# Kernel optimization log

Hardware: AMD Instinct MI355X
Metric: run time of the kernel (lower is better)

Reference implementation:

```python
import jax, jax.numpy as jnp
import numpy as np

DIM = 768
HEADS = 12
HEAD_DIM = DIM // HEADS  # 64, must equal 2*ROPE_DIM
HIDDEN = int(DIM * 4 * 2 / 3)  # 2048
EPS = 1e-6


def _ln(x, w, b, eps=EPS):
    mu = jnp.mean(x, -1, keepdims=True)
    var = jnp.mean((x - mu) ** 2, -1, keepdims=True)
    return (x - mu) * jax.lax.rsqrt(var + eps) * w + b


def _rotate_half(x):
    xr = x.reshape(x.shape[:-1] + (-1, 2))
    return jnp.stack((-xr[..., 1], xr[..., 0]), -1).reshape(x.shape)


def _rope_tables(H, W):
    # Matches get_rope: dim=32 per axis, pt_seq_len=16, theta=10000
    dim, pt, theta = 32, 16.0, 10000.0
    freqs = 1.0 / theta ** (np.arange(0, dim, 2, dtype=np.float32) / dim)  # [16]
    fH = np.repeat((np.arange(H, dtype=np.float32) / H * pt)[:, None] * freqs[None, :], 2, axis=-1)  # [H,32]
    fW = np.repeat((np.arange(W, dtype=np.float32) / W * pt)[:, None] * freqs[None, :], 2, axis=-1)  # [W,32]
    f = np.concatenate([np.broadcast_to(fH[:, None, :], (H, W, dim)),
                        np.broadcast_to(fW[None, :, :], (H, W, dim))], -1)  # [H,W,64]
    f = f.reshape(H * W, 2 * dim)
    return jnp.asarray(np.cos(f)), jnp.asarray(np.sin(f))


def block_forward(x, ln1_w, ln1_b, q_w, q_b, k_w, v_w, v_b, proj_w, proj_b,
                  ln2_w, ln2_b, w1_w, w1_b, w2_w, w2_b, ffn_w, ffn_b, w3_w, w3_b, ws):
    B, H, W, C = x.shape
    shortcut = x
    h = _ln(x, ln1_w, ln1_b)
    # window partition with padding
    pad_h = (-H) % ws
    pad_w = (-W) % ws
    h = jnp.pad(h, ((0, 0), (0, pad_h), (0, pad_w), (0, 0)))
    Hp, Wp = H + pad_h, W + pad_w
    h = h.reshape(B, Hp // ws, ws, Wp // ws, ws, C).transpose(0, 1, 3, 2, 4, 5).reshape(-1, ws, ws, C)
    Bw = h.shape[0]
    N = ws * ws
    t = h.reshape(Bw, N, C)
    q = t @ q_w + q_b  # k has no bias
    k = t @ k_w
    v = t @ v_w + v_b
    q = q.reshape(Bw, N, HEADS, HEAD_DIM).transpose(0, 2, 1, 3)  # [Bw,h,N,d]
    k = k.reshape(Bw, N, HEADS, HEAD_DIM).transpose(0, 2, 1, 3)
    v = v.reshape(Bw, N, HEADS, HEAD_DIM).transpose(0, 2, 1, 3)
    cos, sin = _rope_tables(ws, ws)  # [N, 64]
    q = q * cos + _rotate_half(q) * sin
    k = k * cos + _rotate_half(k) * sin
    scale = HEAD_DIM ** (-0.5)
    attn = jax.nn.softmax(jnp.einsum('bhnd,bhmd->bhnm', q * scale, k), axis=-1)
    o = jnp.einsum('bhnm,bhmd->bhnd', attn, v).transpose(0, 2, 1, 3).reshape(Bw, N, -1)
    o = o @ proj_w + proj_b
    o = o.reshape(Bw, ws, ws, C)
    # window unpartition
    o = o.reshape(B, Hp // ws, Wp // ws, ws, ws, C).transpose(0, 1, 3, 2, 4, 5).reshape(B, Hp, Wp, C)
    o = o[:, :H, :W, :]
    x = shortcut + o
    # SwiGLU MLP with sub-LN
    h = _ln(x, ln2_w, ln2_b)
    hid = jax.nn.silu(h @ w1_w + w1_b) * (h @ w2_w + w2_b)
    hid = _ln(hid, ffn_w, ffn_b)
    return x + hid @ w3_w + w3_b


def setup_inputs() -> dict:
    key = jax.random.key(0)
    ks = jax.random.split(key, 9)
    s = 0.02
    d = {
        'x': jax.random.normal(ks[0], (8, 64, 64, DIM), jnp.float32),
        'ln1_w': jnp.ones((DIM,), jnp.float32),
        'ln1_b': jnp.zeros((DIM,), jnp.float32),
        'q_w': jax.random.normal(ks[1], (DIM, DIM), jnp.float32) * s,
        'q_b': jnp.zeros((DIM,), jnp.float32),
        'k_w': jax.random.normal(ks[2], (DIM, DIM), jnp.float32) * s,
        'v_w': jax.random.normal(ks[3], (DIM, DIM), jnp.float32) * s,
        'v_b': jnp.zeros((DIM,), jnp.float32),
        'proj_w': jax.random.normal(ks[4], (DIM, DIM), jnp.float32) * s,
        'proj_b': jnp.zeros((DIM,), jnp.float32),
        'ln2_w': jnp.ones((DIM,), jnp.float32),
        'ln2_b': jnp.zeros((DIM,), jnp.float32),
        'w1_w': jax.random.normal(ks[5], (DIM, HIDDEN), jnp.float32) * s,
        'w1_b': jnp.zeros((HIDDEN,), jnp.float32),
        'w2_w': jax.random.normal(ks[6], (DIM, HIDDEN), jnp.float32) * s,
        'w2_b': jnp.zeros((HIDDEN,), jnp.float32),
        'ffn_w': jnp.ones((HIDDEN,), jnp.float32),
        'ffn_b': jnp.zeros((HIDDEN,), jnp.float32),
        'w3_w': jax.random.normal(ks[7], (HIDDEN, DIM), jnp.float32) * s,
        'w3_b': jnp.zeros((DIM,), jnp.float32),
        'window_size': 14,
    }
    return d


def reference(x, ln1_w, ln1_b, q_w, q_b, k_w, v_w, v_b, proj_w, proj_b,
              ln2_w, ln2_b, w1_w, w1_b, w2_w, w2_b, ffn_w, ffn_b, w3_w, w3_b, window_size):
    return block_forward(x, ln1_w, ln1_b, q_w, q_b, k_w, v_w, v_b, proj_w, proj_b,
                         ln2_w, ln2_b, w1_w, w1_b, w2_w, w2_b, ffn_w, ffn_b, w3_w, w3_b,
                         int(window_size))
```

## Files before the change

kernel.cpp:

```cpp
#include <hip/hip_runtime.h>
#include <hip/hip_bf16.h>
#include <stdint.h>

typedef unsigned short u16;
typedef unsigned int u32;
typedef __attribute__((ext_vector_type(4))) float f32x4;
typedef __attribute__((ext_vector_type(8))) short s16x8;
typedef __attribute__((ext_vector_type(4))) u32 u32x4;

#define DEV __device__ __forceinline__
#define AS1 __attribute__((address_space(1)))
#define AS3 __attribute__((address_space(3)))

constexpr int T2 = 8 * 64 * 64;
constexpr int C = 768;
constexpr int HID = 2048;
constexpr int CHUNK = 8192;
constexpr int QKVS = 2304;

DEV float blo(u32 u) { return __uint_as_float(u << 16); }
DEV float bhi(u32 u) { return __uint_as_float(u & 0xffff0000u); }
DEV float b2f(u16 u) { return __uint_as_float((u32)u << 16); }
DEV u16 f2bf(float f) {
  u32 x = __float_as_uint(f);
  u32 r = x + 0x7fffu + ((x >> 16) & 1u);
  return (u16)(r >> 16);
}
DEV u32 pack2(float a, float b) { return (u32)f2bf(a) | ((u32)f2bf(b) << 16); }
DEV u32 cvtpk(float lo, float hi) {
  u32 r;
  asm("v_cvt_pk_bf16_f32 %0, %1, %2" : "=v"(r) : "v"(lo), "v"(hi));
  return r;
}

template <int NW>
DEV void reduce2(float& s, float& q) {
#pragma unroll
  for (int o = 32; o > 0; o >>= 1) {
    s += __shfl_down(s, o);
    q += __shfl_down(q, o);
  }
  __shared__ float ps[2 * NW];
  int wave = threadIdx.x >> 6, lane = threadIdx.x & 63;
  if (lane == 0) { ps[wave] = s; ps[NW + wave] = q; }
  __syncthreads();
  s = 0.f; q = 0.f;
#pragma unroll
  for (int i = 0; i < NW; ++i) { s += ps[i]; q += ps[NW + i]; }
}

__global__ __launch_bounds__(256) void transpose_cvt_tiled_k(
    const float* __restrict__ src, u16* __restrict__ dst, int K, int N, int rs, int ro) {
  __shared__ float t[32][33];
  int k0 = blockIdx.x * 32, n0 = blockIdx.y * 32;
  int tx = threadIdx.x, ty = threadIdx.y;
#pragma unroll
  for (int j = 0; j < 4; ++j)
    t[ty + j * 8][tx] = src[(size_t)(k0 + ty + j * 8) * N + n0 + tx];
  __syncthreads();
#pragma unroll
  for (int j = 0; j < 4; ++j) {
    int n = n0 + ty + j * 8;
    dst[((size_t)n * rs + ro) * K + k0 + tx] = f2bf(t[tx][ty + j * 8]);
  }
}

__global__ void build_biases_k(const float* __restrict__ qb, const float* __restrict__ vbb,
                               const float* __restrict__ w1b, const float* __restrict__ w2b,
                               float* __restrict__ qkvb, float* __restrict__ w12b) {
  int i = blockIdx.x * 256 + threadIdx.x;
  if (i < 2304)
    qkvb[i] = i < 768 ? qb[i] : (i < 1536 ? 0.f : vbb[i - 1536]);
  int j = i - 2304;
  if (j >= 0 && j < 4096) w12b[j] = (j & 1) ? w2b[j >> 1] : w1b[j >> 1];
}

__global__ void rope_tables_k(float2* __restrict__ csp) {
  int i = blockIdx.x * 256 + threadIdx.x;
  if (i >= 196 * 32) return;
  int n = i >> 5, dp = i & 31;
  int r = n / 14, c = n - r * 14;
  float pos, fj;
  if (dp < 16) { pos = (float)r * (16.f / 14.f); fj = (float)dp; }
  else         { pos = (float)c * (16.f / 14.f); fj = (float)(dp - 16); }
  float fr = __expf(fj * (-2.f / 32.f) * logf(10000.f));
  float ang = pos * fr;
  csp[i] = make_float2(cosf(ang), sinf(ang));
}

__global__ __launch_bounds__(256) void ln_k(const float* __restrict__ in,
    const float* __restrict__ w, const float* __restrict__ bb, u16* __restrict__ out) {
  size_t row = blockIdx.x;
  int tid = threadIdx.x;
  const float* xr = in + row * C;
  float v0 = xr[tid], v1 = xr[tid + 256], v2 = xr[tid + 512];
  float s = v0 + v1 + v2, q = v0 * v0 + v1 * v1 + v2 * v2;
  reduce2<4>(s, q);
  float mu = s * (1.f / 768.f), var = q * (1.f / 768.f) - mu * mu;
  float rs = rsqrtf(var + 1e-6f);
  u16* orow = out + row * C;
  orow[tid]       = f2bf((v0 - mu) * rs * w[tid]       + bb[tid]);
  orow[tid + 256] = f2bf((v1 - mu) * rs * w[tid + 256] + bb[tid + 256]);
  orow[tid + 512] = f2bf((v2 - mu) * rs * w[tid + 512] + bb[tid + 512]);
}

__global__ __launch_bounds__(384) void ln_bf16_k(const u16* __restrict__ in,
    const float* __restrict__ w, const float* __restrict__ bb, u16* __restrict__ out) {
  size_t row = blockIdx.x;
  int t = threadIdx.x;
  u32 u = ((const u32*)(in + row * C))[t];
  float v0 = blo(u), v1 = bhi(u);
  float s = v0 + v1, q = v0 * v0 + v1 * v1;
  reduce2<6>(s, q);
  float mu = s * (1.f / 768.f), var = q * (1.f / 768.f) - mu * mu;
  float rs = rsqrtf(var + 1e-6f);
  float o0 = (v0 - mu) * rs * w[2 * t] + bb[2 * t];
  float o1 = (v1 - mu) * rs * w[2 * t + 1] + bb[2 * t + 1];
  ((u32*)(out + row * C))[t] = cvtpk(o0, o1);
}

template <int EPI>
__global__ __launch_bounds__(512, 2) void gemm256_k(
    const u16* __restrict__ A, const u16* __restrict__ Bt,
    const float* __restrict__ bias, void* __restrict__ Cout,
    const void* __restrict__ resid, int M, int Nn, int K, int lda,
    const float2* __restrict__ csp) {
  __shared__ u16 LDS[65536];
  const int tid = threadIdx.x;
  const int wave = tid >> 6, lane = tid & 63;
  const int wm = wave >> 2, wn = wave & 3;
  const int l16 = lane & 15, lq = lane >> 4;
  const int gx = gridDim.x;
  const int id = blockIdx.y * gx + blockIdx.x;
  const int xcd = id & 7;
  const int j0 = id >> 3;
  const int W = gx >> 3;
  const int SW = W < 8 ? W : 8;
  const int per_sub = gridDim.y * SW;
  const int sub = j0 / per_sub;
  const int jj = j0 - sub * per_sub;
  const int tm = xcd * W + sub * SW + (jj & (SW - 1));
  const int tn = jj / SW;

  f32x4 acc[8][4];
#pragma unroll
  for (int a = 0; a < 8; ++a)
#pragma unroll
    for (int b = 0; b < 4; ++b)
#pragma unroll
      for (int e = 0; e < 4; ++e) acc[a][b][e] = 0.f;

  const int nk = K >> 6;
  auto STAGE = [&](int kt, int buf) {
    const int k0 = kt << 6;
    u16* Ad = LDS + buf * 32768;
    u16* Bd = Ad + 16384;
#pragma unroll
    for (int i = 0; i < 4; ++i) {
      int blk = (wave << 2) + i;
      int row = (blk << 3) + (lane >> 3);
      int cl = (lane & 7) ^ (row & 7);
      const u16* sa = A + (size_t)(tm * 256 + row) * lda + k0 + cl * 8;
      __builtin_amdgcn_global_load_lds((const AS1 u32*)sa, (AS3 u32*)(Ad + (blk << 9)),
                                       16, 0, 0);
      const u16* sb = Bt + (size_t)(tn * 256 + row) * K + k0 + cl * 8;
      __builtin_amdgcn_global_load_lds((const AS1 u32*)sb, (AS3 u32*)(Bd + (blk << 9)),
                                       16, 0, 0);
    }
  };

  STAGE(0, 0);
  asm volatile("s_waitcnt vmcnt(0)" ::: "memory");
  __syncthreads();
  for (int t = 0; t < nk; ++t) {
    const int cur = t & 1;
    if (t + 1 < nk) STAGE(t + 1, cur ^ 1);
    const u16* As = LDS + cur * 32768;
    const u16* Bs = As + 16384;
#pragma unroll
    for (int ks = 0; ks < 2; ++ks) {
      s16x8 bfr[4];
#pragma unroll
      for (int nf = 0; nf < 4; ++nf) {
        int row = (wn << 6) + (nf << 4) + l16;
        int sc = ((ks << 2) + lq) ^ (row & 7);
        bfr[nf] = *(const s16x8*)(Bs + row * 64 + sc * 8);
      }
      __builtin_amdgcn_s_setprio(1);
#pragma unroll
      for (int mf = 0; mf < 8; ++mf) {
        int row = (wm << 7) + (mf << 4) + l16;
        int sc = ((ks << 2) + lq) ^ (row & 7);
        s16x8 af = *(const s16x8*)(As + row * 64 + sc * 8);
#pragma unroll
        for (int nf = 0; nf < 4; ++nf)
          acc[mf][nf] =
              __builtin_amdgcn_mfma_f32_16x16x32_bf16(af, bfr[nf], acc[mf][nf], 0, 0, 0);
      }
      __builtin_amdgcn_s_setprio(0);
    }
    asm volatile("s_waitcnt vmcnt(0)" ::: "memory");
    __syncthreads();
  }

#pragma unroll
  for (int nf = 0; nf < 4; ++nf) {
    int lcol = (wn << 6) + (nf << 4) + l16;
    int col = (tn << 8) + lcol;
    float bs = bias[col];
#pragma unroll
    for (int mf = 0; mf < 8; ++mf) {
      int rloc = (wm << 7) + (mf << 4) + (lq << 2);
      float v[4];
#pragma unroll
      for (int j = 0; j < 4; ++j) v[j] = acc[mf][nf][j] + bs;
      if constexpr (EPI == 1) {
        const float* rp = (const float*)resid;
#pragma unroll
        for (int j = 0; j < 4; ++j)
          v[j] += rp[(size_t)(tm * 256 + rloc + j) * Nn + col];
      }
#pragma unroll
      for (int j = 0; j < 4; ++j) {
        int row = rloc + j;
        int byte = row * 512 + ((lcol * 2) ^ ((row & 7) << 4));
        *(u16*)((char*)LDS + byte) = f2bf(v[j]);
      }
    }
  }
  __syncthreads();
  u16* Cb = (u16*)Cout + (size_t)(tm * 256) * Nn + (tn << 8);
  const int chunk = tid & 31;
  const int cbase = (tn << 8) + chunk * 8;
  const bool inqk = cbase < 1536, isq = cbase < 768;
  const int dp0 = (cbase & 63) >> 1;
#pragma unroll
  for (int it = 0; it < 16; ++it) {
    int row = (tid >> 5) + it * 16;
    int byte = row * 512 + ((chunk * 16) ^ ((row & 7) << 4));
    u32x4 val = *(const u32x4*)((const char*)LDS + byte);
    if constexpr (EPI == 3) {
      if (inqk) {
        int tok = tm * 256 + row;
        int rem = tok & 4095;
        int n = ((rem >> 6) % 14) * 14 + ((rem & 63) % 14);
        const float2* cp = csp + n * 32 + dp0;
        u32 wv[4] = {val.x, val.y, val.z, val.w};
#pragma unroll
        for (int p = 0; p < 4; ++p) {
          float2 cs = cp[p];
          float e = blo(wv[p]), o = bhi(wv[p]);
          float re = e * cs.x - o * cs.y;
          float ro = o * cs.x + e * cs.y;
          if (isq) { re *= 0.125f; ro *= 0.125f; }
          wv[p] = cvtpk(re, ro);
        }
        val = (u32x4){wv[0], wv[1], wv[2], wv[3]};
      }
    }
    *(u32x4*)(Cb + (size_t)row * Nn + chunk * 8) = val;
  }
}

__global__ __launch_bounds__(256) void gemm_k(
    const u16* __restrict__ A, const u16* __restrict__ Bt,
    const float* __restrict__ bias, float* __restrict__ Cout,
    const u16* __restrict__ resid, int M, int Nn, int K, int lda) {
  __shared__ u16 As[128 * 64];
  __shared__ u16 Bs[128 * 64];
  const int tid = threadIdx.x;
  const int wave = tid >> 6, lane = tid & 63;
  const int wm = wave >> 1, wn = wave & 1;
  const int gx = gridDim.x;
  const int id = blockIdx.y * gx + blockIdx.x;
  const int xcd = id & 7;
  const int j0 = id >> 3;
  const int W = gx >> 3;
  const int SW = W < 8 ? W : 8;
  const int per_sub = gridDim.y * SW;
  const int sub = j0 / per_sub;
  const int jj = j0 - sub * per_sub;
  const int tm = xcd * W + sub * SW + (jj & (SW - 1));
  const int tn = jj / SW;
  const int l16 = lane & 15, lq = lane >> 4;

  f32x4 acc[4][4];
#pragma unroll
  for (int a = 0; a < 4; ++a)
#pragma unroll
    for (int b = 0; b < 4; ++b)
#pragma unroll
      for (int e = 0; e < 4; ++e) acc[a][b][e] = 0.f;

  const int nk = K >> 6;
  for (int kt = 0; kt < nk; ++kt) {
    const int k0 = kt << 6;
#pragma unroll
    for (int i = 0; i < 4; ++i) {
      int row = (((wave << 2) + i) << 3) + (lane >> 3);
      int cl = (lane & 7) ^ (row & 7);
      const u16* sa = A + (size_t)(tm * 128 + row) * lda + k0 + cl * 8;
      __builtin_amdgcn_global_load_lds((const AS1 u32*)sa,
          (AS3 u32*)(As + (((wave << 2) + i) << 9)), 16, 0, 0);
      const u16* sb = Bt + (size_t)(tn * 128 + row) * K + k0 + cl * 8;
      __builtin_amdgcn_global_load_lds((const AS1 u32*)sb,
          (AS3 u32*)(Bs + (((wave << 2) + i) << 9)), 16, 0, 0);
    }
    asm volatile("s_waitcnt vmcnt(0)" ::: "memory");
    __syncthreads();
#pragma unroll
    for (int ks = 0; ks < 2; ++ks) {
      s16x8 af[4], bfr[4];
#pragma unroll
      for (int mf = 0; mf < 4; ++mf) {
        int row = (wm << 6) + (mf << 4) + l16;
        int sc = ((ks << 2) + lq) ^ (row & 7);
        af[mf] = *(const s16x8*)(As + row * 64 + sc * 8);
      }
#pragma unroll
      for (int nf = 0; nf < 4; ++nf) {
        int row = (wn << 6) + (nf << 4) + l16;
        int sc = ((ks << 2) + lq) ^ (row & 7);
        bfr[nf] = *(const s16x8*)(Bs + row * 64 + sc * 8);
      }
      __builtin_amdgcn_s_setprio(1);
#pragma unroll
      for (int mf = 0; mf < 4; ++mf)
#pragma unroll
        for (int nf = 0; nf < 4; ++nf)
          acc[mf][nf] =
              __builtin_amdgcn_mfma_f32_16x16x32_bf16(af[mf], bfr[nf], acc[mf][nf], 0, 0, 0);
      __builtin_amdgcn_s_setprio(0);
    }
    __syncthreads();
  }
#pragma unroll
  for (int nf = 0; nf < 4; ++nf) {
    int col = (tn << 7) + (wn << 6) + (nf << 4) + l16;
    float bs = bias[col];
#pragma unroll
    for (int mf = 0; mf < 4; ++mf) {
      int rbase = (tm << 7) + (wm << 6) + (mf << 4) + (lq << 2);
#pragma unroll
      for (int j = 0; j < 4; ++j) {
        size_t idx = (size_t)(rbase + j) * Nn + col;
        __builtin_nontemporal_store(b2f(resid[idx]) + acc[mf][nf][j] + bs, &Cout[idx]);
      }
    }
  }
}

__global__ __launch_bounds__(256) void attn_mfma_k(u16* __restrict__ qkv,
    const float* __restrict__ vb) {
  __shared__ u16 Vt[64 * 224];
  __shared__ u16 Pl[4 * 16 * 40];
  __shared__ int rowTab[208];
  int wid = blockIdx.x / 12, h = blockIdx.x - wid * 12;
  int bi = wid / 25, wr = wid - bi * 25;
  int hi = wr / 5, wj = wr - hi * 5;
  int rh = (hi == 4) ? 8 : 14, rw = (wj == 4) ? 8 : 14;
  int nv = rh * rw;
  int nk16 = (nv + 15) >> 4;
  int kvfull = nk16 >> 1;
  int nsteps = kvfull + (nk16 & 1);
  int vcols = ((nk16 + 1) >> 1) << 5;
  int tid = threadIdx.x;
  int rowbase = (bi * 64 + hi * 14) * 64 + wj * 14;

  if (tid < 208) {
    int mk = tid < nv ? tid : nv - 1;
    int nr = mk / rw, nc = mk - nr * rw;
    rowTab[tid] = rowbase + nr * 64 + nc;
  }
  __syncthreads();
  for (int idx = tid; idx < vcols * 32; idx += 256) {
    int key = idx >> 5, dp = idx & 31;
    int d = dp << 1;
    u32 val;
    if (key < nv) {
      size_t off = (size_t)rowTab[key] * QKVS + 1536 + (h << 6) + d;
      val = *(const u32*)(qkv + off);
    } else {
      val = pack2(vb[(h << 6) + d], vb[(h << 6) + d + 1]);
    }
    int b0 = (d * 448 + key * 2) ^ ((d & 7) << 4);
    int b1 = ((d + 1) * 448 + key * 2) ^ (((d + 1) & 7) << 4);
    Vt[b0 >> 1] = (u16)(val & 0xffffu);
    Vt[b1 >> 1] = (u16)(val >> 16);
  }
  __syncthreads();

  int wave = tid >> 6, lane = tid & 63;
  int l16 = lane & 15, lq = lane >> 4;
  u16* Pw = Pl + wave * 640;
  const u16* kbase = qkv + 768 + (h << 6);
  float vbr[4];
#pragma unroll
  for (int dt = 0; dt < 4; ++dt) vbr[dt] = vb[(h << 6) + dt * 16 + l16];

  int mtiles = (nv + 15) >> 4;
  for (int mt = wave; mt < mtiles; mt += 4) {
    s16x8 a[2];
    {
      int qi = mt * 16 + l16;
      const u16* qp = qkv + (size_t)rowTab[qi] * QKVS + (h << 6);
      a[0] = *(const s16x8*)(qp + lq * 8);
      a[1] = *(const s16x8*)(qp + 32 + lq * 8);
    }
    f32x4 O[4];
#pragma unroll
    for (int dt = 0; dt < 4; ++dt)
#pragma unroll
      for (int j = 0; j < 4; ++j) O[dt][j] = 0.f;
    float lrow[4] = {0.f, 0.f, 0.f, 0.f};

    for (int kv = 0; kv < nsteps; ++kv) {
      const bool full = kv < kvfull;
      const int keyb = kv << 5;
      f32x4 s0 = {0.f, 0.f, 0.f, 0.f}, s1 = {0.f, 0.f, 0.f, 0.f};
      int key0 = keyb + l16, key1 = key0 + 16;
      const u16* kr0 = kbase + (size_t)rowTab[key0] * QKVS;
      const u16* kr1 = full ? (kbase + (size_t)rowTab[key1] * QKVS) : kbase;
      __builtin_amdgcn_s_setprio(1);
#pragma unroll
      for (int s = 0; s < 2; ++s) {
        s16x8 b0 = *(const s16x8*)(kr0 + s * 32 + lq * 8);
        s0 = __builtin_amdgcn_mfma_f32_16x16x32_bf16(a[s], b0, s0, 0, 0, 0);
        if (full) {
          s16x8 b1 = *(const s16x8*)(kr1 + s * 32 + lq * 8);
          s1 = __builtin_amdgcn_mfma_f32_16x16x32_bf16(a[s], b1, s1, 0, 0, 0);
        }
      }
      __builtin_amdgcn_s_setprio(0);
#pragma unroll
      for (int j = 0; j < 4; ++j) {
        float p0 = key0 < nv ? __expf(s0[j]) : (key0 < 196 ? 1.f : 0.f);
        float p1 = full ? (key1 < nv ? __expf(s1[j]) : (key1 < 196 ? 1.f : 0.f)) : 0.f;
        float rs = p0 + p1;
        rs += __shfl_xor(rs, 1);
        rs += __shfl_xor(rs, 2);
        rs += __shfl_xor(rs, 4);
        rs += __shfl_xor(rs, 8);
        lrow[j] += rs;
        u32 pk = cvtpk(p0, p1);
        Pw[(lq * 4 + j) * 40 + l16] = (u16)pk;
        Pw[(lq * 4 + j) * 40 + l16 + 16] = (u16)(pk >> 16);
      }
      s16x8 pa = *(const s16x8*)(Pw + l16 * 40 + lq * 8);
      __builtin_amdgcn_s_setprio(1);
#pragma unroll
      for (int dt = 0; dt < 4; ++dt) {
        int d = dt * 16 + l16;
        int vbyte = (d * 448 + keyb * 2 + lq * 16) ^ ((d & 7) << 4);
        s16x8 bv = *(const s16x8*)(Vt + (vbyte >> 1));
        O[dt] = __builtin_amdgcn_mfma_f32_16x16x32_bf16(pa, bv, O[dt], 0, 0, 0);
      }
      __builtin_amdgcn_s_setprio(0);
    }
    int Prem = 196 - (nk16 << 4);
    if (Prem > 0) {
#pragma unroll
      for (int j = 0; j < 4; ++j) {
        lrow[j] += (float)Prem;
#pragma unroll
        for (int dt = 0; dt < 4; ++dt) O[dt][j] += (float)Prem * vbr[dt];
      }
    }
#pragma unroll
    for (int j = 0; j < 4; ++j) {
      int qi = mt * 16 + lq * 4 + j;
      if (qi < nv) {
        float inv = 1.f / lrow[j];
        u16* op = qkv + (size_t)rowTab[qi] * QKVS + (h << 6);
#pragma unroll
        for (int dt = 0; dt < 4; ++dt) op[dt * 16 + l16] = f2bf(O[dt][j] * inv);
      }
    }
  }
}

__global__ __launch_bounds__(256) void swiglu_ln_k(u16* __restrict__ h12,
    const float* __restrict__ w, const float* __restrict__ bb) {
  size_t row = blockIdx.x;
  int tid = threadIdx.x;
  const u32x4 ua = *(const u32x4*)(h12 + row * 4096 + tid * 16);
  const u32x4 ub = *(const u32x4*)(h12 + row * 4096 + tid * 16 + 8);
  u32 pp[8] = {ua.x, ua.y, ua.z, ua.w, ub.x, ub.y, ub.z, ub.w};
  float g[8];
  float s = 0.f, qq = 0.f;
#pragma unroll
  for (int j = 0; j < 8; ++j) {
    float a = blo(pp[j]), b = bhi(pp[j]);
    float sl = a / (1.f + __expf(-a));
    g[j] = sl * b;
    s += g[j];
    qq += g[j] * g[j];
  }
  reduce2<4>(s, qq);
  float mu = s * (1.f / 2048.f);
  float var = qq * (1.f / 2048.f) - mu * mu;
  float rs = rsqrtf(var + 1e-6f);
  const float* wp = w + tid * 8;
  const float* bp = bb + tid * 8;
  u32 o4[4];
#pragma unroll
  for (int j = 0; j < 4; ++j) {
    float o0 = (g[2 * j] - mu) * rs * wp[2 * j] + bp[2 * j];
    float o1 = (g[2 * j + 1] - mu) * rs * wp[2 * j + 1] + bp[2 * j + 1];
    o4[j] = cvtpk(o0, o1);
  }
  *(u32x4*)(h12 + row * 4096 + tid * 8) = (u32x4){o4[0], o4[1], o4[2], o4[3]};
}

extern "C" void kernel_launch(void* const* d_in, const int* in_sizes, int n_in,
                              void* d_out, int out_size, void* d_ws, size_t ws_size,
                              hipStream_t stream) {
  const float* x    = (const float*)d_in[0];
  const float* ln1w = (const float*)d_in[1];
  const float* ln1b = (const float*)d_in[2];
  const float* qw   = (const float*)d_in[3];
  const float* qb   = (const float*)d_in[4];
  const float* kw   = (const float*)d_in[5];
  const float* vw   = (const float*)d_in[6];
  const float* vb   = (const float*)d_in[7];
  const float* pw   = (const float*)d_in[8];
  const float* pb   = (const float*)d_in[9];
  const float* ln2w = (const float*)d_in[10];
  const float* ln2b = (const float*)d_in[11];
  const float* w1   = (const float*)d_in[12];
  const float* w1b  = (const float*)d_in[13];
  const float* w2   = (const float*)d_in[14];
  const float* w2b  = (const float*)d_in[15];
  const float* ffw  = (const float*)d_in[16];
  const float* ffb  = (const float*)d_in[17];
  const float* w3   = (const float*)d_in[18];
  const float* w3b  = (const float*)d_in[19];

  char* ws = (char*)d_ws;
  size_t off = 0;
  auto alloc = [&](size_t bytes) -> char* {
    char* p = ws + off;
    off += (bytes + 255) & ~(size_t)255;
    return p;
  };
  u16* qkvwt = (u16*)alloc((size_t)QKVS * 768 * 2);
  u16* pwt   = (u16*)alloc((size_t)768 * 768 * 2);
  u16* w12t  = (u16*)alloc((size_t)4096 * 768 * 2);
  u16* w3t   = (u16*)alloc((size_t)768 * 2048 * 2);
  float* qkvb = (float*)alloc((size_t)QKVS * 4);
  float* w12b = (float*)alloc((size_t)4096 * 4);
  float2* csp = (float2*)alloc((size_t)196 * 32 * 8);
  u16* xw  = (u16*)alloc((size_t)T2 * C * 2);
  u16* qkv = (u16*)alloc((size_t)T2 * QKVS * 2);
  u16* x2b  = xw;
  u16* h2   = qkv;
  u16* h12c = qkv + (size_t)T2 * C;
  float* outp = (float*)d_out;

  dim3 tb(32, 8);
  transpose_cvt_tiled_k<<<dim3(24, 24), tb, 0, stream>>>(qw, qkvwt, 768, 768, 1, 0);
  transpose_cvt_tiled_k<<<dim3(24, 24), tb, 0, stream>>>(kw, qkvwt + (size_t)768 * 768, 768, 768, 1, 0);
  transpose_cvt_tiled_k<<<dim3(24, 24), tb, 0, stream>>>(vw, qkvwt + (size_t)1536 * 768, 768, 768, 1, 0);
  transpose_cvt_tiled_k<<<dim3(24, 24), tb, 0, stream>>>(pw, pwt, 768, 768, 1, 0);
  transpose_cvt_tiled_k<<<dim3(24, 64), tb, 0, stream>>>(w1, w12t, 768, 2048, 2, 0);
  transpose_cvt_tiled_k<<<dim3(24, 64), tb, 0, stream>>>(w2, w12t, 768, 2048, 2, 1);
  transpose_cvt_tiled_k<<<dim3(64, 24), tb, 0, stream>>>(w3, w3t, 2048, 768, 1, 0);
  build_biases_k<<<25, 256, 0, stream>>>(qb, vb, w1b, w2b, qkvb, w12b);
  rope_tables_k<<<25, 256, 0, stream>>>(csp);

  ln_k<<<T2, 256, 0, stream>>>(x, ln1w, ln1b, xw);
  gemm256_k<3><<<dim3(T2 / 256, QKVS / 256), 512, 0, stream>>>(
      xw, qkvwt, qkvb, qkv, nullptr, T2, QKVS, 768, 768, csp);
  attn_mfma_k<<<200 * 12, 256, 0, stream>>>(qkv, vb);
  gemm256_k<1><<<dim3(T2 / 256, 3), 512, 0, stream>>>(
      qkv, pwt, pb, x2b, x, T2, 768, 768, QKVS, nullptr);

  ln_bf16_k<<<T2, 384, 0, stream>>>(x2b, ln2w, ln2b, h2);
  for (int cidx = 0; cidx < T2 / CHUNK; ++cidx) {
    const u16* hrow = h2 + (size_t)cidx * CHUNK * C;
    gemm256_k<0><<<dim3(CHUNK / 256, 16), 512, 0, stream>>>(
        hrow, w12t, w12b, h12c, nullptr, CHUNK, 4096, 768, 768, nullptr);
    swiglu_ln_k<<<CHUNK, 256, 0, stream>>>(h12c, ffw, ffb);
    gemm_k<<<dim3(CHUNK / 128, 6), 256, 0, stream>>>(
        h12c, w3t, w3b, outp + (size_t)cidx * CHUNK * C,
        x2b + (size_t)cidx * CHUNK * C, CHUNK, 768, 2048, 4096);
  }
}
```

Baseline: 924.3 us.

## Drop GEMM double buffering and halve LDS to raise occupancy

The 256x256 GEMM now uses a single LDS buffer instead of double buffering, so shared memory halves. The launch bound asks for four blocks per CU. The epilogue is staged in two 128-row passes to fit the smaller LDS. This gives up overlap between global loads and MFMA compute in the hope of more resident blocks, and risks register spills under the tighter bound.

```diff
diff --git a/kernel.cpp b/kernel.cpp
--- a/kernel.cpp
+++ b/kernel.cpp
@@ -120,12 +120,12 @@
 }
 
 template <int EPI>
-__global__ __launch_bounds__(512, 2) void gemm256_k(
+__global__ __launch_bounds__(512, 4) void gemm256_k(
     const u16* __restrict__ A, const u16* __restrict__ Bt,
     const float* __restrict__ bias, void* __restrict__ Cout,
     const void* __restrict__ resid, int M, int Nn, int K, int lda,
     const float2* __restrict__ csp) {
-  __shared__ u16 LDS[65536];
+  __shared__ u16 LDS[32768];
   const int tid = threadIdx.x;
   const int wave = tid >> 6, lane = tid & 63;
   const int wm = wave >> 2, wn = wave & 3;
@@ -151,32 +151,28 @@
       for (int e = 0; e < 4; ++e) acc[a][b][e] = 0.f;
 
   const int nk = K >> 6;
-  auto STAGE = [&](int kt, int buf) {
-    const int k0 = kt << 6;
-    u16* Ad = LDS + buf * 32768;
-    u16* Bd = Ad + 16384;
-#pragma unroll
-    for (int i = 0; i < 4; ++i) {
-      int blk = (wave << 2) + i;
-      int row = (blk << 3) + (lane >> 3);
-      int cl = (lane & 7) ^ (row & 7);
-      const u16* sa = A + (size_t)(tm * 256 + row) * lda + k0 + cl * 8;
-      __builtin_amdgcn_global_load_lds((const AS1 u32*)sa, (AS3 u32*)(Ad + (blk << 9)),
-                                       16, 0, 0);
-      const u16* sb = Bt + (size_t)(tn * 256 + row) * K + k0 + cl * 8;
-      __builtin_amdgcn_global_load_lds((const AS1 u32*)sb, (AS3 u32*)(Bd + (blk << 9)),
-                                       16, 0, 0);
-    }
-  };
-
-  STAGE(0, 0);
-  asm volatile("s_waitcnt vmcnt(0)" ::: "memory");
-  __syncthreads();
   for (int t = 0; t < nk; ++t) {
-    const int cur = t & 1;
-    if (t + 1 < nk) STAGE(t + 1, cur ^ 1);
-    const u16* As = LDS + cur * 32768;
-    const u16* Bs = As + 16384;
+    const int k0 = t << 6;
+    {
+      u16* Ad = LDS;
+      u16* Bd = LDS + 16384;
+#pragma unroll
+      for (int i = 0; i < 4; ++i) {
+        int blk = (wave << 2) + i;
+        int row = (blk << 3) + (lane >> 3);
+        int cl = (lane & 7) ^ (row & 7);
+        const u16* sa = A + (size_t)(tm * 256 + row) * lda + k0 + cl * 8;
+        __builtin_amdgcn_global_load_lds((const AS1 u32*)sa, (AS3 u32*)(Ad + (blk << 9)),
+                                         16, 0, 0);
+        const u16* sb = Bt + (size_t)(tn * 256 + row) * K + k0 + cl * 8;
+        __builtin_amdgcn_global_load_lds((const AS1 u32*)sb, (AS3 u32*)(Bd + (blk << 9)),
+                                         16, 0, 0);
+      }
+    }
+    asm volatile("s_waitcnt vmcnt(0)" ::: "memory");
+    __syncthreads();
+    const u16* As = LDS;
+    const u16* Bs = LDS + 16384;
 #pragma unroll
     for (int ks = 0; ks < 2; ++ks) {
       s16x8 bfr[4];
@@ -199,66 +195,72 @@
       }
       __builtin_amdgcn_s_setprio(0);
     }
-    asm volatile("s_waitcnt vmcnt(0)" ::: "memory");
     __syncthreads();
   }
 
-#pragma unroll
-  for (int nf = 0; nf < 4; ++nf) {
-    int lcol = (wn << 6) + (nf << 4) + l16;
-    int col = (tn << 8) + lcol;
-    float bs = bias[col];
-#pragma unroll
-    for (int mf = 0; mf < 8; ++mf) {
-      int rloc = (wm << 7) + (mf << 4) + (lq << 2);
-      float v[4];
-#pragma unroll
-      for (int j = 0; j < 4; ++j) v[j] = acc[mf][nf][j] + bs;
-      if constexpr (EPI == 1) {
-        const float* rp = (const float*)resid;
-#pragma unroll
-        for (int j = 0; j < 4; ++j)
-          v[j] += rp[(size_t)(tm * 256 + rloc + j) * Nn + col];
-      }
-#pragma unroll
-      for (int j = 0; j < 4; ++j) {
-        int row = rloc + j;
-        int byte = row * 512 + ((lcol * 2) ^ ((row & 7) << 4));
-        *(u16*)((char*)LDS + byte) = f2bf(v[j]);
-      }
-    }
-  }
-  __syncthreads();
   u16* Cb = (u16*)Cout + (size_t)(tm * 256) * Nn + (tn << 8);
   const int chunk = tid & 31;
   const int cbase = (tn << 8) + chunk * 8;
   const bool inqk = cbase < 1536, isq = cbase < 768;
   const int dp0 = (cbase & 63) >> 1;
 #pragma unroll
-  for (int it = 0; it < 16; ++it) {
-    int row = (tid >> 5) + it * 16;
-    int byte = row * 512 + ((chunk * 16) ^ ((row & 7) << 4));
-    u32x4 val = *(const u32x4*)((const char*)LDS + byte);
-    if constexpr (EPI == 3) {
-      if (inqk) {
-        int tok = tm * 256 + row;
-        int rem = tok & 4095;
-        int n = ((rem >> 6) % 14) * 14 + ((rem & 63) % 14);
-        const float2* cp = csp + n * 32 + dp0;
-        u32 wv[4] = {val.x, val.y, val.z, val.w};
-#pragma unroll
-        for (int p = 0; p < 4; ++p) {
-          float2 cs = cp[p];
-          float e = blo(wv[p]), o = bhi(wv[p]);
-          float re = e * cs.x - o * cs.y;
-          float ro = o * cs.x + e * cs.y;
-          if (isq) { re *= 0.125f; ro *= 0.125f; }
-          wv[p] = cvtpk(re, ro);
+  for (int pass = 0; pass < 2; ++pass) {
+    if (wm == pass) {
+#pragma unroll
+      for (int nf = 0; nf < 4; ++nf) {
+        int lcol = (wn << 6) + (nf << 4) + l16;
+        int col = (tn << 8) + lcol;
+        float bs = bias[col];
+#pragma unroll
+        for (int mf = 0; mf < 8; ++mf) {
+          int lrow = (mf << 4) + (lq << 2);
+          float v[4];
+#pragma unroll
+          for (int j = 0; j < 4; ++j) v[j] = acc[mf][nf][j] + bs;
+          if constexpr (EPI == 1) {
+            const float* rp = (const float*)resid;
+#pragma unroll
+            for (int j = 0; j < 4; ++j)
+              v[j] += rp[(size_t)(tm * 256 + (pass << 7) + lrow + j) * Nn + col];
+          }
+#pragma unroll
+          for (int j = 0; j < 4; ++j) {
+            int r = lrow + j;
+            int byte = r * 512 + ((lcol * 2) ^ ((r & 7) << 4));
+            *(u16*)((char*)LDS + byte) = f2bf(v[j]);
+          }
         }
-        val = (u32x4){wv[0], wv[1], wv[2], wv[3]};
-      }
-    }
-    *(u32x4*)(Cb + (size_t)row * Nn + chunk * 8) = val;
+      }
+    }
+    __syncthreads();
+#pragma unroll
+    for (int it = 0; it < 8; ++it) {
+      int lrow = (tid >> 5) + it * 16;
+      int row = (pass << 7) + lrow;
+      int byte = lrow * 512 + ((chunk * 16) ^ ((lrow & 7) << 4));
+      u32x4 val = *(const u32x4*)((const char*)LDS + byte);
+      if constexpr (EPI == 3) {
+        if (inqk) {
+          int tok = tm * 256 + row;
+          int rem = tok & 4095;
+          int n = ((rem >> 6) % 14) * 14 + ((rem & 63) % 14);
+          const float2* cp = csp + n * 32 + dp0;
+          u32 wv[4] = {val.x, val.y, val.z, val.w};
+#pragma unroll
+          for (int p = 0; p < 4; ++p) {
+            float2 cs = cp[p];
+            float e = blo(wv[p]), o = bhi(wv[p]);
+            float re = e * cs.x - o * cs.y;
+            float ro = o * cs.x + e * cs.y;
+            if (isq) { re *= 0.125f; ro *= 0.125f; }
+            wv[p] = cvtpk(re, ro);
+          }
+          val = (u32x4){wv[0], wv[1], wv[2], wv[3]};
+        }
+      }
+      *(u32x4*)(Cb + (size_t)row * Nn + chunk * 8) = val;
+    }
+    if (pass == 0) __syncthreads();
   }
 }
 
```

Measured after the change: 3.505 ms. 3.79x slower.

## Process two query tiles per wave in window attention to reuse K/V loads

Applied to the files above, without the earlier changes.

Each wave now handles two 16-row query tiles at once (mt and mt+4), sharing each loaded K fragment and V fragment across both tiles' MFMAs. A second per-wave P scratch buffer is added in shared memory. This halves the global K loads and LDS V reads per query tile and gives more independent MFMAs to interleave. The cost is more registers, more LDS, and possible load imbalance, since with up to 13 tiles per window some waves now do two tiles while others idle.

```diff
diff --git a/kernel.cpp b/kernel.cpp
--- a/kernel.cpp
+++ b/kernel.cpp
@@ -353,7 +353,7 @@
 __global__ __launch_bounds__(256) void attn_mfma_k(u16* __restrict__ qkv,
     const float* __restrict__ vb) {
   __shared__ u16 Vt[64 * 224];
-  __shared__ u16 Pl[4 * 16 * 40];
+  __shared__ u16 Pl[8 * 16 * 40];
   __shared__ int rowTab[208];
   int wid = blockIdx.x / 12, h = blockIdx.x - wid * 12;
   int bi = wid / 25, wr = wid - bi * 25;
@@ -392,32 +392,42 @@
 
   int wave = tid >> 6, lane = tid & 63;
   int l16 = lane & 15, lq = lane >> 4;
-  u16* Pw = Pl + wave * 640;
+  u16* Pw0 = Pl + wave * 640;
+  u16* Pw1 = Pl + (4 + wave) * 640;
   const u16* kbase = qkv + 768 + (h << 6);
   float vbr[4];
 #pragma unroll
   for (int dt = 0; dt < 4; ++dt) vbr[dt] = vb[(h << 6) + dt * 16 + l16];
+  int Prem = 196 - (nk16 << 4);
 
   int mtiles = (nv + 15) >> 4;
-  for (int mt = wave; mt < mtiles; mt += 4) {
-    s16x8 a[2];
+  for (int mt = wave; mt < mtiles; mt += 8) {
+    const int mtB = mt + 4;
+    const bool hasB = mtB < mtiles;
+    s16x8 a0[2], a1[2];
     {
-      int qi = mt * 16 + l16;
-      const u16* qp = qkv + (size_t)rowTab[qi] * QKVS + (h << 6);
-      a[0] = *(const s16x8*)(qp + lq * 8);
-      a[1] = *(const s16x8*)(qp + 32 + lq * 8);
-    }
-    f32x4 O[4];
+      int qiA = mt * 16 + l16;
+      const u16* qp = qkv + (size_t)rowTab[qiA] * QKVS + (h << 6);
+      a0[0] = *(const s16x8*)(qp + lq * 8);
+      a0[1] = *(const s16x8*)(qp + 32 + lq * 8);
+      int qiB = mtB * 16 + l16;
+      if (qiB > 207) qiB = 207;
+      const u16* qp1 = qkv + (size_t)rowTab[qiB] * QKVS + (h << 6);
+      a1[0] = *(const s16x8*)(qp1 + lq * 8);
+      a1[1] = *(const s16x8*)(qp1 + 32 + lq * 8);
+    }
+    f32x4 O0[4], O1[4];
 #pragma unroll
     for (int dt = 0; dt < 4; ++dt)
 #pragma unroll
-      for (int j = 0; j < 4; ++j) O[dt][j] = 0.f;
-    float lrow[4] = {0.f, 0.f, 0.f, 0.f};
+      for (int j = 0; j < 4; ++j) { O0[dt][j] = 0.f; O1[dt][j] = 0.f; }
+    float l0[4] = {0.f, 0.f, 0.f, 0.f}, l1[4] = {0.f, 0.f, 0.f, 0.f};
 
     for (int kv = 0; kv < nsteps; ++kv) {
       const bool full = kv < kvfull;
       const int keyb = kv << 5;
-      f32x4 s0 = {0.f, 0.f, 0.f, 0.f}, s1 = {0.f, 0.f, 0.f, 0.f};
+      f32x4 sA0 = {0.f, 0.f, 0.f, 0.f}, sA1 = {0.f, 0.f, 0.f, 0.f};
+      f32x4 sB0 = {0.f, 0.f, 0.f, 0.f}, sB1 = {0.f, 0.f, 0.f, 0.f};
       int key0 = keyb + l16, key1 = key0 + 16;
       const u16* kr0 = kbase + (size_t)rowTab[key0] * QKVS;
       const u16* kr1 = full ? (kbase + (size_t)rowTab[key1] * QKVS) : kbase;
@@ -425,55 +435,88 @@
 #pragma unroll
       for (int s = 0; s < 2; ++s) {
         s16x8 b0 = *(const s16x8*)(kr0 + s * 32 + lq * 8);
-        s0 = __builtin_amdgcn_mfma_f32_16x16x32_bf16(a[s], b0, s0, 0, 0, 0);
+        sA0 = __builtin_amdgcn_mfma_f32_16x16x32_bf16(a0[s], b0, sA0, 0, 0, 0);
+        if (hasB) sB0 = __builtin_amdgcn_mfma_f32_16x16x32_bf16(a1[s], b0, sB0, 0, 0, 0);
         if (full) {
           s16x8 b1 = *(const s16x8*)(kr1 + s * 32 + lq * 8);
-          s1 = __builtin_amdgcn_mfma_f32_16x16x32_bf16(a[s], b1, s1, 0, 0, 0);
+          sA1 = __builtin_amdgcn_mfma_f32_16x16x32_bf16(a0[s], b1, sA1, 0, 0, 0);
+          if (hasB) sB1 = __builtin_amdgcn_mfma_f32_16x16x32_bf16(a1[s], b1, sB1, 0, 0, 0);
         }
       }
       __builtin_amdgcn_s_setprio(0);
 #pragma unroll
       for (int j = 0; j < 4; ++j) {
-        float p0 = key0 < nv ? __expf(s0[j]) : (key0 < 196 ? 1.f : 0.f);
-        float p1 = full ? (key1 < nv ? __expf(s1[j]) : (key1 < 196 ? 1.f : 0.f)) : 0.f;
+        float p0 = key0 < nv ? __expf(sA0[j]) : (key0 < 196 ? 1.f : 0.f);
+        float p1 = full ? (key1 < nv ? __expf(sA1[j]) : (key1 < 196 ? 1.f : 0.f)) : 0.f;
         float rs = p0 + p1;
         rs += __shfl_xor(rs, 1);
         rs += __shfl_xor(rs, 2);
         rs += __shfl_xor(rs, 4);
         rs += __shfl_xor(rs, 8);
-        lrow[j] += rs;
+        l0[j] += rs;
         u32 pk = cvtpk(p0, p1);
-        Pw[(lq * 4 + j) * 40 + l16] = (u16)pk;
-        Pw[(lq * 4 + j) * 40 + l16 + 16] = (u16)(pk >> 16);
-      }
-      s16x8 pa = *(const s16x8*)(Pw + l16 * 40 + lq * 8);
+        Pw0[(lq * 4 + j) * 40 + l16] = (u16)pk;
+        Pw0[(lq * 4 + j) * 40 + l16 + 16] = (u16)(pk >> 16);
+      }
+      if (hasB) {
+#pragma unroll
+        for (int j = 0; j < 4; ++j) {
+          float p0 = key0 < nv ? __expf(sB0[j]) : (key0 < 196 ? 1.f : 0.f);
+          float p1 = full ? (key1 < nv ? __expf(sB1[j]) : (key1 < 196 ? 1.f : 0.f)) : 0.f;
+          float rs = p0 + p1;
+          rs += __shfl_xor(rs, 1);
+          rs += __shfl_xor(rs, 2);
+          rs += __shfl_xor(rs, 4);
+          rs += __shfl_xor(rs, 8);
+          l1[j] += rs;
+          u32 pk = cvtpk(p0, p1);
+          Pw1[(lq * 4 + j) * 40 + l16] = (u16)pk;
+          Pw1[(lq * 4 + j) * 40 + l16 + 16] = (u16)(pk >> 16);
+        }
+      }
+      s16x8 pa0 = *(const s16x8*)(Pw0 + l16 * 40 + lq * 8);
+      s16x8 pa1;
+      if (hasB) pa1 = *(const s16x8*)(Pw1 + l16 * 40 + lq * 8);
       __builtin_amdgcn_s_setprio(1);
 #pragma unroll
       for (int dt = 0; dt < 4; ++dt) {
         int d = dt * 16 + l16;
         int vbyte = (d * 448 + keyb * 2 + lq * 16) ^ ((d & 7) << 4);
         s16x8 bv = *(const s16x8*)(Vt + (vbyte >> 1));
-        O[dt] = __builtin_amdgcn_mfma_f32_16x16x32_bf16(pa, bv, O[dt], 0, 0, 0);
+        O0[dt] = __builtin_amdgcn_mfma_f32_16x16x32_bf16(pa0, bv, O0[dt], 0, 0, 0);
+        if (hasB) O1[dt] = __builtin_amdgcn_mfma_f32_16x16x32_bf16(pa1, bv, O1[dt], 0, 0, 0);
       }
       __builtin_amdgcn_s_setprio(0);
     }
-    int Prem = 196 - (nk16 << 4);
     if (Prem > 0) {
 #pragma unroll
       for (int j = 0; j < 4; ++j) {
-        lrow[j] += (float)Prem;
-#pragma unroll
-        for (int dt = 0; dt < 4; ++dt) O[dt][j] += (float)Prem * vbr[dt];
+        l0[j] += (float)Prem;
+        l1[j] += (float)Prem;
+#pragma unroll
+        for (int dt = 0; dt < 4; ++dt) {
+          O0[dt][j] += (float)Prem * vbr[dt];
+          O1[dt][j] += (float)Prem * vbr[dt];
+        }
       }
     }
 #pragma unroll
     for (int j = 0; j < 4; ++j) {
-      int qi = mt * 16 + lq * 4 + j;
-      if (qi < nv) {
-        float inv = 1.f / lrow[j];
-        u16* op = qkv + (size_t)rowTab[qi] * QKVS + (h << 6);
-#pragma unroll
-        for (int dt = 0; dt < 4; ++dt) op[dt * 16 + l16] = f2bf(O[dt][j] * inv);
+      int qiA = mt * 16 + lq * 4 + j;
+      if (qiA < nv) {
+        float inv = 1.f / l0[j];
+        u16* op = qkv + (size_t)rowTab[qiA] * QKVS + (h << 6);
+#pragma unroll
+        for (int dt = 0; dt < 4; ++dt) op[dt * 16 + l16] = f2bf(O0[dt][j] * inv);
+      }
+      if (hasB) {
+        int qiB = mtB * 16 + lq * 4 + j;
+        if (qiB < nv) {
+          float inv = 1.f / l1[j];
+          u16* op = qkv + (size_t)rowTab[qiB] * QKVS + (h << 6);
+#pragma unroll
+          for (int dt = 0; dt < 4; ++dt) op[dt * 16 + l16] = f2bf(O1[dt][j] * inv);
+        }
       }
     }
   }
```

Measured after the change: 954.3 us. 1.03x slower.
